# Performance work log

Measured on AMD Instinct MI355X. Metric: run time of the kernel, lower is better.

## Reference

```python
import jax, jax.numpy as jnp
import numpy as np

N = 100000   # nodes
E = 3200000  # edges (avg degree 32)
F_IN = 128   # node feature dim (lazy in_channels)
C = 16       # GAT out_channels, heads=1
ED = 2       # edge_dim
B = 512      # graphs in batch
OUT_X = 64; OUT_Y = 64; ROT = 4
EPS = 1e-5


def _bn(x, g, b):
    # BatchNorm1d in training mode: biased batch variance, eps=1e-5
    mu = x.mean(0, keepdims=True)
    var = x.var(0, keepdims=True)
    return g * (x - mu) * jax.lax.rsqrt(var + EPS) + b


def _gat(x, src, dst, edge_attr, W, We, att_s, att_d, att_e, bias):
    # PyG GATConv, heads=1: self-loops added with fill_value='mean' edge attrs
    n = x.shape[0]
    deg = jax.ops.segment_sum(jnp.ones_like(dst, jnp.float32), dst, num_segments=n)
    loop_attr = jax.ops.segment_sum(edge_attr, dst, num_segments=n) / jnp.maximum(deg, 1.0)[:, None]
    idx = jnp.arange(n)
    src_f = jnp.concatenate([src, idx])
    dst_f = jnp.concatenate([dst, idx])
    ea = jnp.concatenate([edge_attr, loop_attr], axis=0)  # [E+N, ED]
    h = x @ W                      # [N, C]
    a_s = h @ att_s                # [N]
    a_d = h @ att_d                # [N]
    a_e = (ea @ We) @ att_e        # [E+N]
    logits = jax.nn.leaky_relu(a_s[src_f] + a_d[dst_f] + a_e, 0.2)
    m = jax.ops.segment_max(logits, dst_f, num_segments=n)  # every node has a self-loop
    ex = jnp.exp(logits - m[dst_f])
    alpha = ex / jax.ops.segment_sum(ex, dst_f, num_segments=n)[dst_f]
    return jax.ops.segment_sum(alpha[:, None] * h[src_f], dst_f, num_segments=n) + bias


def _glorot(k, shp):
    lim = float(np.sqrt(6.0 / (shp[0] + shp[1])))
    return jax.random.uniform(k, shp, jnp.float32, -lim, lim)


def setup_inputs() -> dict:
    key = jax.random.key(0)
    k = jax.random.split(key, 48)
    d = {}
    d['x'] = jax.random.normal(k[0], (N, F_IN), jnp.float32)
    d['edge_index'] = jax.random.randint(k[1], (2, E), 0, N)
    d['edge_attr'] = jax.random.normal(k[2], (E, ED), jnp.float32)
    d['batch'] = jnp.sort(jax.random.randint(k[3], (N,), 0, B))
    # gat1
    d['W1'] = _glorot(k[4], (F_IN, C)); d['We1'] = _glorot(k[5], (ED, C))
    d['as1'] = 0.1 * jax.random.normal(k[6], (C,)); d['ad1'] = 0.1 * jax.random.normal(k[7], (C,))
    d['ae1'] = 0.1 * jax.random.normal(k[8], (C,)); d['b1'] = jnp.zeros((C,), jnp.float32)
    # norm1 (BatchNorm on nodes)
    d['g1'] = 1.0 + 0.1 * jax.random.normal(k[9], (C,)); d['bb1'] = 0.1 * jax.random.normal(k[10], (C,))
    # gat2
    d['W2'] = _glorot(k[11], (C, C)); d['We2'] = _glorot(k[12], (ED, C))
    d['as2'] = 0.1 * jax.random.normal(k[13], (C,)); d['ad2'] = 0.1 * jax.random.normal(k[14], (C,))
    d['ae2'] = 0.1 * jax.random.normal(k[15], (C,)); d['b2'] = jnp.zeros((C,), jnp.float32)
    # D2RL MLP tail
    d['gL1'] = 1.0 + 0.1 * jax.random.normal(k[16], (C,)); d['bL1'] = 0.1 * jax.random.normal(k[17], (C,))
    d['Wl1'] = _glorot(k[18], (C, C)); d['bl1'] = 0.1 * jax.random.normal(k[19], (C,))
    d['gL2'] = 1.0 + 0.1 * jax.random.normal(k[20], (2 * C,)); d['bL2'] = 0.1 * jax.random.normal(k[21], (2 * C,))
    d['Wl2'] = _glorot(k[22], (2 * C, C)); d['bl2'] = 0.1 * jax.random.normal(k[23], (C,))
    d['gL3'] = 1.0 + 0.1 * jax.random.normal(k[24], (2 * C,)); d['bL3'] = 0.1 * jax.random.normal(k[25], (2 * C,))
    d['Wl3'] = _glorot(k[26], (2 * C, C)); d['bl3'] = 0.1 * jax.random.normal(k[27], (C,))
    d['Wx'] = _glorot(k[28], (C, OUT_X)); d['bx'] = 0.1 * jax.random.normal(k[29], (OUT_X,))
    d['Wy'] = _glorot(k[30], (C, OUT_Y)); d['by'] = 0.1 * jax.random.normal(k[31], (OUT_Y,))
    d['Wr'] = _glorot(k[32], (C, ROT)); d['br'] = 0.1 * jax.random.normal(k[33], (ROT,))
    return d


def reference(x, edge_index, edge_attr, batch,
              W1, We1, as1, ad1, ae1, b1, g1, bb1,
              W2, We2, as2, ad2, ae2, b2,
              gL1, bL1, Wl1, bl1, gL2, bL2, Wl2, bl2, gL3, bL3, Wl3, bl3,
              Wx, bx, Wy, by, Wr, br):
    src, dst = edge_index[0], edge_index[1]
    h = jax.nn.relu(_gat(x, src, dst, edge_attr, W1, We1, as1, ad1, ae1, b1))
    h = _bn(h, g1, bb1)
    h = jax.nn.relu(_gat(h, src, dst, edge_attr, W2, We2, as2, ad2, ae2, b2))
    # MeanAggregation over graphs
    cnt = jax.ops.segment_sum(jnp.ones((h.shape[0],), jnp.float32), batch, num_segments=B)
    xe = jax.ops.segment_sum(h, batch, num_segments=B) / jnp.maximum(cnt, 1.0)[:, None]  # [B, C]
    z = _bn(xe, gL1, bL1)
    z = jax.nn.relu(z @ Wl1 + bl1)
    z = _bn(jnp.concatenate([z, xe], axis=1), gL2, bL2)
    z = jax.nn.relu(z @ Wl2 + bl2)
    z = _bn(jnp.concatenate([z, xe], axis=1), gL3, bL3)
    z = jax.nn.relu(z @ Wl3 + bl3)
    xx = jax.nn.softmax(z @ Wx + bx, axis=1)
    y = jax.nn.softmax(z @ Wy + by, axis=1)
    rot = jax.nn.softmax(z @ Wr + br, axis=1)
    return (xx, y, rot)
```

## Files before the change

kernel.cpp:

```cpp
#include <hip/hip_runtime.h>
#include <hip/hip_fp16.h>
#include <math.h>

#define C 16
#define FIN 128

typedef unsigned int u32x2 __attribute__((ext_vector_type(2)));

__global__ __launch_bounds__(256) void k_gemm1(
    const float* __restrict__ x, const float* __restrict__ W,
    const float* __restrict__ asw, const float* __restrict__ adw,
    __half* __restrict__ hh, float* __restrict__ a_s, float* __restrict__ a_d, int n) {
  __shared__ float xs[64 * 129];
  __shared__ float Ws[FIN * C];
  __shared__ float pAs[4][64], pAd[4][64];
  int t = threadIdx.x;
  int node0 = blockIdx.x * 64;
  for (int i = t; i < FIN * C; i += 256) Ws[i] = W[i];
  for (int i = t; i < 64 * FIN; i += 256) {
    int r = i >> 7, c = i & 127;
    int node = node0 + r;
    xs[r * 129 + c] = (node < n) ? x[(size_t)node * FIN + c] : 0.f;
  }
  __syncthreads();
  int nn = t & 63, cg = (t >> 6) * 4, grp = t >> 6;
  float a0 = 0.f, a1 = 0.f, a2 = 0.f, a3 = 0.f;
  const float* xr = &xs[nn * 129];
  #pragma unroll 8
  for (int k = 0; k < FIN; ++k) {
    float xv = xr[k];
    const float* wr = &Ws[k * C + cg];
    a0 += xv * wr[0]; a1 += xv * wr[1]; a2 += xv * wr[2]; a3 += xv * wr[3];
  }
  int node = node0 + nn;
  if (node < n) {
    __half2 p0 = __floats2half2_rn(a0, a1), p1 = __floats2half2_rn(a2, a3);
    unsigned u0, u1;
    memcpy(&u0, &p0, 4); memcpy(&u1, &p1, 4);
    *(uint2*)(hh + (size_t)node * 16 + cg) = make_uint2(u0, u1);
  }
  pAs[grp][nn] = a0 * asw[cg] + a1 * asw[cg + 1] + a2 * asw[cg + 2] + a3 * asw[cg + 3];
  pAd[grp][nn] = a0 * adw[cg] + a1 * adw[cg + 1] + a2 * adw[cg + 2] + a3 * adw[cg + 3];
  __syncthreads();
  if (t < 64 && node0 + t < n) {
    a_s[node0 + t] = pAs[0][t] + pAs[1][t] + pAs[2][t] + pAs[3][t];
    a_d[node0 + t] = pAd[0][t] + pAd[1][t] + pAd[2][t] + pAd[3][t];
  }
}

__global__ __launch_bounds__(256) void k_hist_rank(
    const int* __restrict__ dst, int* __restrict__ counts,
    int* __restrict__ rank, int ne) {
  int e = blockIdx.x * 256 + threadIdx.x;
  if (e < ne) rank[e] = atomicAdd(&counts[dst[e]], 1);
}

__global__ __launch_bounds__(512) void k_scan1(const int* __restrict__ counts,
                                               int* __restrict__ bsum, int n) {
  __shared__ int sd[512];
  int i = blockIdx.x * 512 + threadIdx.x;
  sd[threadIdx.x] = (i < n) ? counts[i] : 0;
  __syncthreads();
  for (int s = 256; s > 0; s >>= 1) {
    if (threadIdx.x < s) sd[threadIdx.x] += sd[threadIdx.x + s];
    __syncthreads();
  }
  if (threadIdx.x == 0) bsum[blockIdx.x] = sd[0];
}

__global__ __launch_bounds__(512) void k_scan2(int* __restrict__ bsum,
                                               int* __restrict__ offs,
                                               int nblk, int n) {
  __shared__ int sd[512];
  int t = threadIdx.x;
  int v = (t < nblk) ? bsum[t] : 0;
  sd[t] = v;
  __syncthreads();
  for (int off = 1; off < 512; off <<= 1) {
    int x = (t >= off) ? sd[t - off] : 0;
    __syncthreads();
    sd[t] += x;
    __syncthreads();
  }
  if (t < nblk) bsum[t] = sd[t] - v;
  if (t == nblk - 1) offs[n] = sd[t];
}

__global__ __launch_bounds__(512) void k_scan3(const int* __restrict__ counts,
                                               const int* __restrict__ bsum,
                                               int* __restrict__ offs, int n) {
  __shared__ int sd[512];
  int t = threadIdx.x;
  int i = blockIdx.x * 512 + t;
  int v = (i < n) ? counts[i] : 0;
  sd[t] = v;
  __syncthreads();
  for (int off = 1; off < 512; off <<= 1) {
    int x = (t >= off) ? sd[t - off] : 0;
    __syncthreads();
    sd[t] += x;
    __syncthreads();
  }
  if (i < n) offs[i] = bsum[blockIdx.x] + sd[t] - v;
}

__global__ __launch_bounds__(256) void k_scatter(
    const int* __restrict__ src, const int* __restrict__ dst,
    const float2* __restrict__ ea, const int* __restrict__ offs,
    const int* __restrict__ rank,
    const float* __restrict__ We1, const float* __restrict__ ae1,
    const float* __restrict__ We2, const float* __restrict__ ae2,
    uint2* __restrict__ bucket, int ne) {
  int e = blockIdx.x * 256 + threadIdx.x;
  if (e >= ne) return;
  float w01 = 0.f, w11 = 0.f, w02 = 0.f, w12 = 0.f;
  #pragma unroll
  for (int c = 0; c < C; ++c) {
    w01 += We1[c] * ae1[c]; w11 += We1[C + c] * ae1[c];
    w02 += We2[c] * ae2[c]; w12 += We2[C + c] * ae2[c];
  }
  int d = dst[e];
  float2 a = ea[e];
  __half2 hp = __floats2half2_rn(a.x * w01 + a.y * w11, a.x * w02 + a.y * w12);
  unsigned hb;
  memcpy(&hb, &hp, 4);
  bucket[offs[d] + rank[e]] = make_uint2((unsigned)src[e], hb);
}

__global__ __launch_bounds__(256) void k_gather(
    const uint2* __restrict__ bucket, const int* __restrict__ offs,
    const float* __restrict__ a_s, const float* __restrict__ a_d,
    const __half* __restrict__ hh, const float* __restrict__ bias,
    float* __restrict__ outv, float* __restrict__ bnsum, float* __restrict__ bnsq,
    int lay, int do_bn, int n) {
  __shared__ float sbn[32];
  int t = threadIdx.x;
  if (do_bn) {
    if (t < 32) sbn[t] = 0.f;
    __syncthreads();
  }

  int node = blockIdx.x * 32 + (t >> 3);
  int l = t & 7, f = l & 1, p = l >> 1;

  float acc[8];
  #pragma unroll
  for (int j = 0; j < 8; ++j) acc[j] = 0.f;
  float den = 0.f, ssum = 0.f;
  int o0 = 0, o1 = 0;
  float adi = 0.f, asi = 0.f;
  if (node < n) {
    o0 = offs[node]; o1 = offs[node + 1];
    adi = a_d[node]; asi = a_s[node];
    int e = o0 + p;
    u32x2 r = {0u, 0u};
    if (e < o1) r = __builtin_nontemporal_load((const u32x2*)(bucket + e));
    while (e < o1) {
      int en = e + 4;
      u32x2 rn = {0u, 0u};
      if (en < o1) rn = __builtin_nontemporal_load((const u32x2*)(bucket + en));
      int s = (int)r.x;
      unsigned scb = r.y;
      __half2 sc2;
      memcpy(&sc2, &scb, 4);
      float se = lay ? __high2float(sc2) : __low2float(sc2);
      float asv = a_s[s];
      uint4 hv = *(const uint4*)(hh + ((size_t)s << 4) + (f << 3));
      float lg = asv + adi + se;
      lg = lg > 0.f ? lg : 0.2f * lg;
      float ex = __expf(lg);
      den += ex; ssum += se;
      __half2 t0, t1, t2, t3;
      memcpy(&t0, &hv.x, 4); memcpy(&t1, &hv.y, 4);
      memcpy(&t2, &hv.z, 4); memcpy(&t3, &hv.w, 4);
      float2 g0 = __half22float2(t0), g1 = __half22float2(t1);
      float2 g2 = __half22float2(t2), g3 = __half22float2(t3);
      acc[0] += ex * g0.x; acc[1] += ex * g0.y;
      acc[2] += ex * g1.x; acc[3] += ex * g1.y;
      acc[4] += ex * g2.x; acc[5] += ex * g2.y;
      acc[6] += ex * g3.x; acc[7] += ex * g3.y;
      r = rn; e = en;
    }
  }
  #pragma unroll
  for (int off = 2; off <= 4; off <<= 1) {
    den += __shfl_xor(den, off);
    ssum += __shfl_xor(ssum, off);
    #pragma unroll
    for (int j = 0; j < 8; ++j) acc[j] += __shfl_xor(acc[j], off);
  }

  float v[8];
  #pragma unroll
  for (int j = 0; j < 8; ++j) v[j] = 0.f;
  if (node < n) {
    float dgc = fmaxf((float)(o1 - o0), 1.f);
    float lg = asi + adi + ssum / dgc;
    lg = lg > 0.f ? lg : 0.2f * lg;
    float exs = __expf(lg);
    uint4 hv = *(const uint4*)(hh + ((size_t)node << 4) + (f << 3));
    __half2 t0, t1, t2, t3;
    memcpy(&t0, &hv.x, 4); memcpy(&t1, &hv.y, 4);
    memcpy(&t2, &hv.z, 4); memcpy(&t3, &hv.w, 4);
    float2 g0 = __half22float2(t0), g1 = __half22float2(t1);
    float2 g2 = __half22float2(t2), g3 = __half22float2(t3);
    float hs[8] = {g0.x, g0.y, g1.x, g1.y, g2.x, g2.y, g3.x, g3.y};
    float inv = 1.f / (den + exs);
    const float* bp = bias + f * 8;
    #pragma unroll
    for (int j = 0; j < 8; ++j)
      v[j] = fmaxf((acc[j] + exs * hs[j]) * inv + bp[j], 0.f);
    if (p == 0) {
      float4* op = (float4*)(outv + ((size_t)node << 4));
      op[f * 2]     = make_float4(v[0], v[1], v[2], v[3]);
      op[f * 2 + 1] = make_float4(v[4], v[5], v[6], v[7]);
    }
  }

  if (do_bn) {
    float sv[8], qv[8];
    bool act = (node < n) && (p == 0);
    #pragma unroll
    for (int j = 0; j < 8; ++j) {
      sv[j] = act ? v[j] : 0.f;
      qv[j] = sv[j] * sv[j];
    }
    #pragma unroll
    for (int j = 0; j < 8; ++j) {
      sv[j] += __shfl_down(sv[j], 8);  qv[j] += __shfl_down(qv[j], 8);
      sv[j] += __shfl_down(sv[j], 16); qv[j] += __shfl_down(qv[j], 16);
      sv[j] += __shfl_down(sv[j], 32); qv[j] += __shfl_down(qv[j], 32);
    }
    if ((t & 63) < 2) {
      #pragma unroll
      for (int j = 0; j < 8; ++j) {
        atomicAdd(&sbn[f * 8 + j], sv[j]);
        atomicAdd(&sbn[16 + f * 8 + j], qv[j]);
      }
    }
    __syncthreads();
    if (t < 16) atomicAdd(&bnsum[t], sbn[t]);
    else if (t < 32) atomicAdd(&bnsq[t - 16], sbn[t]);
  }
}

__global__ void k_bnp(const float* __restrict__ bnsum, const float* __restrict__ bnsq,
                      const float* __restrict__ g, const float* __restrict__ bb,
                      float* __restrict__ scale, float* __restrict__ shift, float invn) {
  int c = threadIdx.x;
  if (c >= C) return;
  float mean = bnsum[c] * invn;
  float var = bnsq[c] * invn - mean * mean;
  float s = g[c] * rsqrtf(var + 1e-5f);
  scale[c] = s; shift[c] = bb[c] - mean * s;
}

__global__ __launch_bounds__(256) void k_node2(
    const float* __restrict__ outv, const float* __restrict__ scale,
    const float* __restrict__ shift, const float* __restrict__ W2,
    const float* __restrict__ asw, const float* __restrict__ adw,
    __half* __restrict__ hh, float* __restrict__ a_s, float* __restrict__ a_d, int n) {
  __shared__ float w2s[C * C];
  if (threadIdx.x < C * C) w2s[threadIdx.x] = W2[threadIdx.x];
  __syncthreads();
  int i = blockIdx.x * 256 + threadIdx.x;
  if (i >= n) return;
  float hn[C];
  #pragma unroll
  for (int c = 0; c < C; ++c) hn[c] = outv[(size_t)i * C + c] * scale[c] + shift[c];
  float h2[C];
  #pragma unroll
  for (int j = 0; j < C; ++j) {
    float acc = 0.f;
    #pragma unroll
    for (int c = 0; c < C; ++c) acc += hn[c] * w2s[c * C + j];
    h2[j] = acc;
  }
  float hs = 0.f, hd = 0.f;
  #pragma unroll
  for (int j = 0; j < C; ++j) { hs += h2[j] * asw[j]; hd += h2[j] * adw[j]; }
  a_s[i] = hs; a_d[i] = hd;
  unsigned wbits[8];
  #pragma unroll
  for (int j = 0; j < 8; ++j) {
    __half2 hq = __floats2half2_rn(h2[2 * j], h2[2 * j + 1]);
    memcpy(&wbits[j], &hq, 4);
  }
  uint4* hp = (uint4*)(hh + (size_t)i * 16);
  hp[0] = make_uint4(wbits[0], wbits[1], wbits[2], wbits[3]);
  hp[1] = make_uint4(wbits[4], wbits[5], wbits[6], wbits[7]);
}

__global__ void k_gstart(const int* __restrict__ batch, int* __restrict__ gs,
                         int n, int B_) {
  int g = blockIdx.x * blockDim.x + threadIdx.x;
  if (g > B_) return;
  if (g == B_) { gs[B_] = n; return; }
  int lo = 0, hi = n;
  while (lo < hi) { int mid = (lo + hi) >> 1; if (batch[mid] < g) lo = mid + 1; else hi = mid; }
  gs[g] = lo;
}

__global__ __launch_bounds__(256) void k_xe(
    const float* __restrict__ outv, const int* __restrict__ gs,
    float* __restrict__ xe, int B_) {
  int wave = blockIdx.x * 4 + (threadIdx.x >> 6);
  if (wave >= B_) return;
  int lane = threadIdx.x & 63;
  int c = lane & 15, sub = lane >> 4;
  int base = gs[wave], end = gs[wave + 1];
  float s = 0.f;
  for (int n0 = base + sub; n0 < end; n0 += 4) s += outv[(size_t)n0 * C + c];
  s += __shfl_down(s, 32);
  s += __shfl_down(s, 16);
  if (lane < 16) xe[(size_t)wave * C + c] = s / fmaxf((float)(end - base), 1.f);
}

__global__ __launch_bounds__(512) void k_tail_z3(
    const float* __restrict__ xe_in,
    const float* __restrict__ gL1, const float* __restrict__ bL1,
    const float* __restrict__ Wl1, const float* __restrict__ bl1,
    const float* __restrict__ gL2, const float* __restrict__ bL2,
    const float* __restrict__ Wl2, const float* __restrict__ bl2,
    const float* __restrict__ gL3, const float* __restrict__ bL3,
    const float* __restrict__ Wl3, const float* __restrict__ bl3,
    float* __restrict__ z3buf, int B_) {
  __shared__ float ssum[2 * C], ssq[2 * C], sc[2 * C], sh[2 * C];
  int t = threadIdx.x;
  float invB = 1.f / (float)B_;
  float xe[C];
  #pragma unroll
  for (int c = 0; c < C; ++c) xe[c] = xe_in[(size_t)t * C + c];

  if (t < 2 * C) { ssum[t] = 0.f; ssq[t] = 0.f; }
  __syncthreads();
  #pragma unroll
  for (int c = 0; c < C; ++c) {
    float s = xe[c], q = xe[c] * xe[c];
    for (int o = 32; o > 0; o >>= 1) { s += __shfl_down(s, o); q += __shfl_down(q, o); }
    if ((t & 63) == 0) { atomicAdd(&ssum[c], s); atomicAdd(&ssq[c], q); }
  }
  __syncthreads();
  if (t < C) {
    float mean = ssum[t] * invB, var = ssq[t] * invB - mean * mean;
    float s = gL1[t] * rsqrtf(var + 1e-5f);
    sc[t] = s; sh[t] = bL1[t] - mean * s;
  }
  __syncthreads();
  float z[C];
  #pragma unroll
  for (int j = 0; j < C; ++j) {
    float acc = bl1[j];
    #pragma unroll
    for (int c = 0; c < C; ++c) acc += (xe[c] * sc[c] + sh[c]) * Wl1[c * C + j];
    z[j] = fmaxf(acc, 0.f);
  }
  __syncthreads();

  if (t < 2 * C) { ssum[t] = 0.f; ssq[t] = 0.f; }
  __syncthreads();
  #pragma unroll
  for (int c = 0; c < C; ++c) {
    float s = z[c], q = z[c] * z[c];
    for (int o = 32; o > 0; o >>= 1) { s += __shfl_down(s, o); q += __shfl_down(q, o); }
    if ((t & 63) == 0) { atomicAdd(&ssum[c], s); atomicAdd(&ssq[c], q); }
    float s2 = xe[c], q2 = xe[c] * xe[c];
    for (int o = 32; o > 0; o >>= 1) { s2 += __shfl_down(s2, o); q2 += __shfl_down(q2, o); }
    if ((t & 63) == 0) { atomicAdd(&ssum[C + c], s2); atomicAdd(&ssq[C + c], q2); }
  }
  __syncthreads();
  if (t < 2 * C) {
    float mean = ssum[t] * invB, var = ssq[t] * invB - mean * mean;
    float s = gL2[t] * rsqrtf(var + 1e-5f);
    sc[t] = s; sh[t] = bL2[t] - mean * s;
  }
  __syncthreads();
  float z2[C];
  #pragma unroll
  for (int j = 0; j < C; ++j) {
    float acc = bl2[j];
    #pragma unroll
    for (int c = 0; c < C; ++c) acc += (z[c] * sc[c] + sh[c]) * Wl2[c * C + j];
    #pragma unroll
    for (int c = 0; c < C; ++c) acc += (xe[c] * sc[C + c] + sh[C + c]) * Wl2[(C + c) * C + j];
    z2[j] = fmaxf(acc, 0.f);
  }
  __syncthreads();

  if (t < 2 * C) { ssum[t] = 0.f; ssq[t] = 0.f; }
  __syncthreads();
  #pragma unroll
  for (int c = 0; c < C; ++c) {
    float s = z2[c], q = z2[c] * z2[c];
    for (int o = 32; o > 0; o >>= 1) { s += __shfl_down(s, o); q += __shfl_down(q, o); }
    if ((t & 63) == 0) { atomicAdd(&ssum[c], s); atomicAdd(&ssq[c], q); }
    float s2 = xe[c], q2 = xe[c] * xe[c];
    for (int o = 32; o > 0; o >>= 1) { s2 += __shfl_down(s2, o); q2 += __shfl_down(q2, o); }
    if ((t & 63) == 0) { atomicAdd(&ssum[C + c], s2); atomicAdd(&ssq[C + c], q2); }
  }
  __syncthreads();
  if (t < 2 * C) {
    float mean = ssum[t] * invB, var = ssq[t] * invB - mean * mean;
    float s = gL3[t] * rsqrtf(var + 1e-5f);
    sc[t] = s; sh[t] = bL3[t] - mean * s;
  }
  __syncthreads();
  #pragma unroll
  for (int j = 0; j < C; ++j) {
    float acc = bl3[j];
    #pragma unroll
    for (int c = 0; c < C; ++c) acc += (z2[c] * sc[c] + sh[c]) * Wl3[c * C + j];
    #pragma unroll
    for (int c = 0; c < C; ++c) acc += (xe[c] * sc[C + c] + sh[C + c]) * Wl3[(C + c) * C + j];
    z3buf[(size_t)t * C + j] = fmaxf(acc, 0.f);
  }
}

__global__ __launch_bounds__(256) void k_heads(
    const float* __restrict__ z3buf,
    const float* __restrict__ Wx, const float* __restrict__ bx,
    const float* __restrict__ Wy, const float* __restrict__ by,
    const float* __restrict__ Wr, const float* __restrict__ br,
    float* __restrict__ out, int B_) {
  int wv = blockIdx.x * 4 + (threadIdx.x >> 6);
  if (wv >= B_) return;
  int lane = threadIdx.x & 63;
  float z[C];
  #pragma unroll
  for (int c = 0; c < C; ++c) z[c] = z3buf[(size_t)wv * C + c];

  float ax = bx[lane];
  #pragma unroll
  for (int c = 0; c < C; ++c) ax += z[c] * Wx[c * 64 + lane];
  float m = ax;
  #pragma unroll
  for (int o = 32; o > 0; o >>= 1) m = fmaxf(m, __shfl_xor(m, o));
  float e = __expf(ax - m);
  float s = e;
  #pragma unroll
  for (int o = 32; o > 0; o >>= 1) s += __shfl_xor(s, o);
  out[(size_t)wv * 64 + lane] = e / s;

  float ay = by[lane];
  #pragma unroll
  for (int c = 0; c < C; ++c) ay += z[c] * Wy[c * 64 + lane];
  m = ay;
  #pragma unroll
  for (int o = 32; o > 0; o >>= 1) m = fmaxf(m, __shfl_xor(m, o));
  e = __expf(ay - m);
  s = e;
  #pragma unroll
  for (int o = 32; o > 0; o >>= 1) s += __shfl_xor(s, o);
  out[(size_t)B_ * 64 + (size_t)wv * 64 + lane] = e / s;

  if (lane < 4) {
    float ar = br[lane];
    #pragma unroll
    for (int c = 0; c < C; ++c) ar += z[c] * Wr[c * 4 + lane];
    float mr = ar;
    mr = fmaxf(mr, __shfl_xor(mr, 1));
    mr = fmaxf(mr, __shfl_xor(mr, 2));
    float er = __expf(ar - mr);
    float sr = er;
    sr += __shfl_xor(sr, 1);
    sr += __shfl_xor(sr, 2);
    out[(size_t)B_ * 128 + (size_t)wv * 4 + lane] = er / sr;
  }
}

extern "C" void kernel_launch(void* const* d_in, const int* in_sizes, int n_in,
                              void* d_out, int out_size, void* d_ws, size_t ws_size,
                              hipStream_t stream) {
  const float* x     = (const float*)d_in[0];
  const int*   eidx  = (const int*)d_in[1];
  const float* eattr = (const float*)d_in[2];
  const int*   batch = (const int*)d_in[3];
  const float* W1  = (const float*)d_in[4];
  const float* We1 = (const float*)d_in[5];
  const float* as1 = (const float*)d_in[6];
  const float* ad1 = (const float*)d_in[7];
  const float* ae1 = (const float*)d_in[8];
  const float* b1  = (const float*)d_in[9];
  const float* g1  = (const float*)d_in[10];
  const float* bb1 = (const float*)d_in[11];
  const float* W2  = (const float*)d_in[12];
  const float* We2 = (const float*)d_in[13];
  const float* as2 = (const float*)d_in[14];
  const float* ad2 = (const float*)d_in[15];
  const float* ae2 = (const float*)d_in[16];
  const float* b2  = (const float*)d_in[17];
  const float* gL1 = (const float*)d_in[18];
  const float* bL1 = (const float*)d_in[19];
  const float* Wl1 = (const float*)d_in[20];
  const float* bl1 = (const float*)d_in[21];
  const float* gL2 = (const float*)d_in[22];
  const float* bL2 = (const float*)d_in[23];
  const float* Wl2 = (const float*)d_in[24];
  const float* bl2 = (const float*)d_in[25];
  const float* gL3 = (const float*)d_in[26];
  const float* bL3 = (const float*)d_in[27];
  const float* Wl3 = (const float*)d_in[28];
  const float* bl3 = (const float*)d_in[29];
  const float* Wx  = (const float*)d_in[30];
  const float* bx  = (const float*)d_in[31];
  const float* Wy  = (const float*)d_in[32];
  const float* by  = (const float*)d_in[33];
  const float* Wr  = (const float*)d_in[34];
  const float* br  = (const float*)d_in[35];

  int N = in_sizes[3];
  int E = in_sizes[2] / 2;
  int B = out_size / 132;
  int nblk = (N + 511) / 512;

  char* w = (char*)d_ws;
  size_t o = 0;
  auto alloc = [&](size_t bytes) { char* p = w + o; o += (bytes + 15) & ~15ull; return p; };
  uint2*  bucket = (uint2*)alloc((size_t)E * 8);
  int*    rank   = (int*)alloc((size_t)E * 4);
  __half* hh     = (__half*)alloc((size_t)N * C * 2);
  float*  outv   = (float*)alloc((size_t)N * C * 4);
  float*  a_s    = (float*)alloc((size_t)N * 4);
  float*  a_d    = (float*)alloc((size_t)N * 4);
  int*    counts = (int*)alloc((size_t)N * 4);
  int*    offs   = (int*)alloc((size_t)(N + 4) * 4);
  int*    bsum   = (int*)alloc((size_t)(nblk + 4) * 4);
  float*  bn     = (float*)alloc(64 * 4);
  float*  xe     = (float*)alloc((size_t)B * C * 4);
  int*    gs     = (int*)alloc((size_t)(B + 4) * 4);
  float*  z3buf  = (float*)alloc((size_t)B * C * 4);

  const int* src = eidx;
  const int* dst = eidx + E;
  int ebl = (E + 255) / 256;
  int nbl = (N + 255) / 256;

  hipMemsetAsync(counts, 0, (size_t)N * 4, stream);
  hipMemsetAsync(bn, 0, 32 * 4, stream);

  k_gemm1<<<(N + 63) / 64, 256, 0, stream>>>(x, W1, as1, ad1, hh, a_s, a_d, N);
  k_hist_rank<<<ebl, 256, 0, stream>>>(dst, counts, rank, E);
  k_scan1<<<nblk, 512, 0, stream>>>(counts, bsum, N);
  k_scan2<<<1, 512, 0, stream>>>(bsum, offs, nblk, N);
  k_scan3<<<nblk, 512, 0, stream>>>(counts, bsum, offs, N);
  k_scatter<<<ebl, 256, 0, stream>>>(src, dst, (const float2*)eattr, offs, rank,
                                     We1, ae1, We2, ae2, bucket, E);
  k_gather<<<(N + 31) / 32, 256, 0, stream>>>(bucket, offs, a_s, a_d, hh, b1,
                                              outv, bn, bn + 16, 0, 1, N);
  k_bnp<<<1, 64, 0, stream>>>(bn, bn + 16, g1, bb1, bn + 32, bn + 48, 1.f / (float)N);
  k_node2<<<nbl, 256, 0, stream>>>(outv, bn + 32, bn + 48, W2, as2, ad2, hh, a_s, a_d, N);
  k_gather<<<(N + 31) / 32, 256, 0, stream>>>(bucket, offs, a_s, a_d, hh, b2,
                                              outv, bn, bn + 16, 1, 0, N);
  k_gstart<<<(B + 1 + 255) / 256, 256, 0, stream>>>(batch, gs, N, B);
  k_xe<<<(B + 3) / 4, 256, 0, stream>>>(outv, gs, xe, B);
  k_tail_z3<<<1, B, 0, stream>>>(xe, gL1, bL1, Wl1, bl1, gL2, bL2, Wl2, bl2,
                                 gL3, bL3, Wl3, bl3, z3buf, B);
  k_heads<<<(B + 3) / 4, 256, 0, stream>>>(z3buf, Wx, bx, Wy, by, Wr, br,
                                           (float*)d_out, B);
}
```

Measured before the change: 712.5 us.

## Replace atomic CSR build with two-pass LDS radix partition; shrink gather lanes per node

Builds the dst-sorted edge bucket with a two-level counting sort. The first pass bins edges by dst>>8 using per-chunk shared-memory histograms and a scan. The second pass sorts each bin by the low 8 bits in shared memory and also writes the offsets. This replaces the global per-edge atomicAdd ranking and the random scatter, at the cost of an extra E-sized temporary buffer and an extra pass over the edges. Separately, the gather now uses 4 lanes per node instead of 8 (64 nodes per block), which cuts shuffle reductions per node but halves per-node edge parallelism.

```diff
diff --git a/kernel.cpp b/kernel.cpp
--- a/kernel.cpp
+++ b/kernel.cpp
@@ -48,13 +48,6 @@
   }
 }
 
-__global__ __launch_bounds__(256) void k_hist_rank(
-    const int* __restrict__ dst, int* __restrict__ counts,
-    int* __restrict__ rank, int ne) {
-  int e = blockIdx.x * 256 + threadIdx.x;
-  if (e < ne) rank[e] = atomicAdd(&counts[dst[e]], 1);
-}
-
 __global__ __launch_bounds__(512) void k_scan1(const int* __restrict__ counts,
                                                int* __restrict__ bsum, int n) {
   __shared__ int sd[512];
@@ -102,6 +95,92 @@
     __syncthreads();
   }
   if (i < n) offs[i] = bsum[blockIdx.x] + sd[t] - v;
+}
+
+
+__global__ __launch_bounds__(256) void k_p1count(
+    const int* __restrict__ dst, int* __restrict__ histT,
+    int ne, int chunk, int G, int nbin) {
+  __shared__ int hist[512];
+  int g = blockIdx.x, t = threadIdx.x;
+  for (int i = t; i < nbin; i += 256) hist[i] = 0;
+  __syncthreads();
+  int e0 = g * chunk, e1 = e0 + chunk; if (e1 > ne) e1 = ne;
+  for (int e = e0 + t; e < e1; e += 256) atomicAdd(&hist[dst[e] >> 8], 1);
+  __syncthreads();
+  for (int i = t; i < nbin; i += 256) histT[i * G + g] = hist[i];
+}
+
+__global__ __launch_bounds__(256) void k_p1scat(
+    const int* __restrict__ src, const int* __restrict__ dst,
+    const float2* __restrict__ ea, const int* __restrict__ histS,
+    const float* __restrict__ We1, const float* __restrict__ ae1,
+    const float* __restrict__ We2, const float* __restrict__ ae2,
+    uint2* __restrict__ tmpR, int* __restrict__ tmpD,
+    int ne, int chunk, int G, int nbin) {
+  __shared__ int cur[512];
+  int g = blockIdx.x, t = threadIdx.x;
+  for (int i = t; i < nbin; i += 256) cur[i] = histS[i * G + g];
+  float w01 = 0.f, w11 = 0.f, w02 = 0.f, w12 = 0.f;
+  #pragma unroll
+  for (int c = 0; c < C; ++c) {
+    w01 += We1[c] * ae1[c]; w11 += We1[C + c] * ae1[c];
+    w02 += We2[c] * ae2[c]; w12 += We2[C + c] * ae2[c];
+  }
+  __syncthreads();
+  int e0 = g * chunk, e1 = e0 + chunk; if (e1 > ne) e1 = ne;
+  for (int e = e0 + t; e < e1; e += 256) {
+    int d = dst[e];
+    int pos = atomicAdd(&cur[d >> 8], 1);
+    float2 a = ea[e];
+    __half2 hp = __floats2half2_rn(a.x * w01 + a.y * w11, a.x * w02 + a.y * w12);
+    unsigned hb;
+    memcpy(&hb, &hp, 4);
+    tmpR[pos] = make_uint2((unsigned)src[e], hb);
+    tmpD[pos] = d;
+  }
+}
+
+__global__ __launch_bounds__(256) void k_p2(
+    const uint2* __restrict__ tmpR, const int* __restrict__ tmpD,
+    const int* __restrict__ histS,
+    uint2* __restrict__ bucket, int* __restrict__ offs,
+    int G, int nbin, int n, int ne) {
+  __shared__ int hist[256], scn[256], cur[256];
+  int b = blockIdx.x, t = threadIdx.x;
+  int cs0 = histS[b * G];
+  int cs1 = (b + 1 < nbin) ? histS[(b + 1) * G] : ne;
+  hist[t] = 0;
+  __syncthreads();
+  for (int i = cs0 + t; i < cs1; i += 256) atomicAdd(&hist[tmpD[i] & 255], 1);
+  __syncthreads();
+  int v = hist[t];
+  scn[t] = v;
+  __syncthreads();
+  for (int off = 1; off < 256; off <<= 1) {
+    int x = (t >= off) ? scn[t - off] : 0;
+    __syncthreads();
+    scn[t] += x;
+    __syncthreads();
+  }
+  int excl = scn[t] - v;
+  int node = b * 256 + t;
+  if (node <= n) offs[node] = cs0 + excl;
+  if (b == 0 && t == 0) offs[n] = ne;
+  cur[t] = cs0 + excl;
+  __syncthreads();
+  for (int i = cs0 + t; i < cs1; i += 256) {
+    int d = tmpD[i];
+    int pos = atomicAdd(&cur[d & 255], 1);
+    bucket[pos] = tmpR[i];
+  }
+}
+
+__global__ __launch_bounds__(256) void k_hist_rank(
+    const int* __restrict__ dst, int* __restrict__ counts,
+    int* __restrict__ rank, int ne) {
+  int e = blockIdx.x * 256 + threadIdx.x;
+  if (e < ne) rank[e] = atomicAdd(&counts[dst[e]], 1);
 }
 
 __global__ __launch_bounds__(256) void k_scatter(
@@ -140,8 +219,8 @@
     __syncthreads();
   }
 
-  int node = blockIdx.x * 32 + (t >> 3);
-  int l = t & 7, f = l & 1, p = l >> 1;
+  int node = blockIdx.x * 64 + (t >> 2);
+  int l = t & 3, f = l & 1, p = l >> 1;
 
   float acc[8];
   #pragma unroll
@@ -156,7 +235,7 @@
     u32x2 r = {0u, 0u};
     if (e < o1) r = __builtin_nontemporal_load((const u32x2*)(bucket + e));
     while (e < o1) {
-      int en = e + 4;
+      int en = e + 2;
       u32x2 rn = {0u, 0u};
       if (en < o1) rn = __builtin_nontemporal_load((const u32x2*)(bucket + en));
       int s = (int)r.x;
@@ -182,13 +261,10 @@
       r = rn; e = en;
     }
   }
-  #pragma unroll
-  for (int off = 2; off <= 4; off <<= 1) {
-    den += __shfl_xor(den, off);
-    ssum += __shfl_xor(ssum, off);
-    #pragma unroll
-    for (int j = 0; j < 8; ++j) acc[j] += __shfl_xor(acc[j], off);
-  }
+  den += __shfl_xor(den, 2);
+  ssum += __shfl_xor(ssum, 2);
+  #pragma unroll
+  for (int j = 0; j < 8; ++j) acc[j] += __shfl_xor(acc[j], 2);
 
   float v[8];
   #pragma unroll
@@ -227,6 +303,7 @@
     }
     #pragma unroll
     for (int j = 0; j < 8; ++j) {
+      sv[j] += __shfl_down(sv[j], 4);  qv[j] += __shfl_down(qv[j], 4);
       sv[j] += __shfl_down(sv[j], 8);  qv[j] += __shfl_down(qv[j], 8);
       sv[j] += __shfl_down(sv[j], 16); qv[j] += __shfl_down(qv[j], 16);
       sv[j] += __shfl_down(sv[j], 32); qv[j] += __shfl_down(qv[j], 32);
@@ -511,45 +588,69 @@
   int N = in_sizes[3];
   int E = in_sizes[2] / 2;
   int B = out_size / 132;
-  int nblk = (N + 511) / 512;
+
+  const int* src = eidx;
+  const int* dst = eidx + E;
+
+  const int G = 256;
+  int nbin = (N + 255) >> 8;
+  int nscan = nbin * G;
+  int chunk = (E + G - 1) / G;
+  int nblk2 = (nscan + 511) / 512;
 
   char* w = (char*)d_ws;
   size_t o = 0;
   auto alloc = [&](size_t bytes) { char* p = w + o; o += (bytes + 15) & ~15ull; return p; };
   uint2*  bucket = (uint2*)alloc((size_t)E * 8);
-  int*    rank   = (int*)alloc((size_t)E * 4);
+  uint2*  tmpR   = (uint2*)alloc((size_t)E * 8);
+  int*    tmpD   = (int*)alloc((size_t)E * 4);
   __half* hh     = (__half*)alloc((size_t)N * C * 2);
   float*  outv   = (float*)alloc((size_t)N * C * 4);
   float*  a_s    = (float*)alloc((size_t)N * 4);
   float*  a_d    = (float*)alloc((size_t)N * 4);
-  int*    counts = (int*)alloc((size_t)N * 4);
   int*    offs   = (int*)alloc((size_t)(N + 4) * 4);
-  int*    bsum   = (int*)alloc((size_t)(nblk + 4) * 4);
+  int*    histT  = (int*)alloc((size_t)(nscan + 4) * 4);
+  int*    histS  = (int*)alloc((size_t)(nscan + 4) * 4);
+  int*    bsum   = (int*)alloc((size_t)(nblk2 + 516) * 4);
   float*  bn     = (float*)alloc(64 * 4);
   float*  xe     = (float*)alloc((size_t)B * C * 4);
   int*    gs     = (int*)alloc((size_t)(B + 4) * 4);
   float*  z3buf  = (float*)alloc((size_t)B * C * 4);
-
-  const int* src = eidx;
-  const int* dst = eidx + E;
-  int ebl = (E + 255) / 256;
+  size_t need_radix = o;
+
+  bool radix = (need_radix <= ws_size) && (nbin <= 512) && (nblk2 <= 512);
+
+  hipMemsetAsync(bn, 0, 32 * 4, stream);
+  k_gemm1<<<(N + 63) / 64, 256, 0, stream>>>(x, W1, as1, ad1, hh, a_s, a_d, N);
+
+  if (radix) {
+    k_p1count<<<G, 256, 0, stream>>>(dst, histT, E, chunk, G, nbin);
+    k_scan1<<<nblk2, 512, 0, stream>>>(histT, bsum, nscan);
+    k_scan2<<<1, 512, 0, stream>>>(bsum, histS, nblk2, nscan);
+    k_scan3<<<nblk2, 512, 0, stream>>>(histT, bsum, histS, nscan);
+    k_p1scat<<<G, 256, 0, stream>>>(src, dst, (const float2*)eattr, histS,
+                                    We1, ae1, We2, ae2, tmpR, tmpD, E, chunk, G, nbin);
+    k_p2<<<nbin, 256, 0, stream>>>(tmpR, tmpD, histS, bucket, offs, G, nbin, N, E);
+  } else {
+    int* rank   = (int*)tmpR;
+    int* counts = (int*)tmpD;
+    int nblk = (N + 511) / 512;
+    int ebl = (E + 255) / 256;
+    hipMemsetAsync(counts, 0, (size_t)N * 4, stream);
+    k_hist_rank<<<ebl, 256, 0, stream>>>(dst, counts, rank, E);
+    k_scan1<<<nblk, 512, 0, stream>>>(counts, bsum, N);
+    k_scan2<<<1, 512, 0, stream>>>(bsum, offs, nblk, N);
+    k_scan3<<<nblk, 512, 0, stream>>>(counts, bsum, offs, N);
+    k_scatter<<<ebl, 256, 0, stream>>>(src, dst, (const float2*)eattr, offs, rank,
+                                       We1, ae1, We2, ae2, bucket, E);
+  }
+
   int nbl = (N + 255) / 256;
-
-  hipMemsetAsync(counts, 0, (size_t)N * 4, stream);
-  hipMemsetAsync(bn, 0, 32 * 4, stream);
-
-  k_gemm1<<<(N + 63) / 64, 256, 0, stream>>>(x, W1, as1, ad1, hh, a_s, a_d, N);
-  k_hist_rank<<<ebl, 256, 0, stream>>>(dst, counts, rank, E);
-  k_scan1<<<nblk, 512, 0, stream>>>(counts, bsum, N);
-  k_scan2<<<1, 512, 0, stream>>>(bsum, offs, nblk, N);
-  k_scan3<<<nblk, 512, 0, stream>>>(counts, bsum, offs, N);
-  k_scatter<<<ebl, 256, 0, stream>>>(src, dst, (const float2*)eattr, offs, rank,
-                                     We1, ae1, We2, ae2, bucket, E);
-  k_gather<<<(N + 31) / 32, 256, 0, stream>>>(bucket, offs, a_s, a_d, hh, b1,
+  k_gather<<<(N + 63) / 64, 256, 0, stream>>>(bucket, offs, a_s, a_d, hh, b1,
                                               outv, bn, bn + 16, 0, 1, N);
   k_bnp<<<1, 64, 0, stream>>>(bn, bn + 16, g1, bb1, bn + 32, bn + 48, 1.f / (float)N);
   k_node2<<<nbl, 256, 0, stream>>>(outv, bn + 32, bn + 48, W2, as2, ad2, hh, a_s, a_d, N);
-  k_gather<<<(N + 31) / 32, 256, 0, stream>>>(bucket, offs, a_s, a_d, hh, b2,
+  k_gather<<<(N + 63) / 64, 256, 0, stream>>>(bucket, offs, a_s, a_d, hh, b2,
                                               outv, bn, bn + 16, 1, 0, N);
   k_gstart<<<(B + 1 + 255) / 256, 256, 0, stream>>>(batch, gs, N, B);
   k_xe<<<(B + 3) / 4, 256, 0, stream>>>(outv, gs, xe, B);
```

New measurement: 672.8 us. 1.06x faster.
